# Kernel tuning notes

Measured on AMD Instinct MI355X. Metric: run time of the kernel, lower is better.

Reference implementation:

```python
import jax, jax.numpy as jnp
import numpy as np
from jax import lax

G = 128          # graphs per batch
N_PER = 512      # nodes per graph (uniform -> static top-k shapes)
N = G * N_PER    # 65536 total nodes
E = 1_048_576    # total edges (8192 per graph)
IN, D, OUT = 256, 128, 16
BN_EPS = 1e-5


def setup_inputs() -> dict:
    key = jax.random.key(0)
    ks = jax.random.split(key, 20)
    e_per = E // G
    off = (jnp.arange(G, dtype=jnp.int32) * N_PER)[:, None]
    src = (off + jax.random.randint(ks[0], (G, e_per), 0, N_PER, dtype=jnp.int32)).reshape(-1)
    dst = (off + jax.random.randint(ks[1], (G, e_per), 0, N_PER, dtype=jnp.int32)).reshape(-1)
    inp = {
        "x": jax.random.normal(ks[2], (N, IN), dtype=jnp.float32),
        "edge_index": jnp.stack([src, dst]),
        "batch": jnp.repeat(jnp.arange(G, dtype=jnp.int32), N_PER),
        # GraphConv1: lin_rel (with bias) + lin_root (no bias)
        "w_rel1": jax.random.normal(ks[3], (IN, D)) / np.sqrt(IN),
        "b_rel1": jnp.zeros((D,), jnp.float32),
        "w_root1": jax.random.normal(ks[4], (IN, D)) / np.sqrt(IN),
        "pool1_w": jax.random.normal(ks[5], (D,)) / np.sqrt(D),
        "w_rel2": jax.random.normal(ks[6], (D, D)) / np.sqrt(D),
        "b_rel2": jnp.zeros((D,), jnp.float32),
        "w_root2": jax.random.normal(ks[7], (D, D)) / np.sqrt(D),
        "pool2_w": jax.random.normal(ks[8], (D,)) / np.sqrt(D),
        "lin1_w": jax.random.normal(ks[9], (2 * D, D)) / np.sqrt(2 * D),
        "lin1_b": jnp.zeros((D,), jnp.float32),
        "bn_gamma": jnp.ones((D,), jnp.float32),
        "bn_beta": jnp.zeros((D,), jnp.float32),
        "bn_mean": jnp.zeros((D,), jnp.float32),
        "bn_var": jnp.ones((D,), jnp.float32),
        "lin2_w": jax.random.normal(ks[10], (D, OUT)) / np.sqrt(D),
        "lin2_b": jnp.zeros((OUT,), jnp.float32),
    }
    return inp


def _graph_conv(x, src, dst, valid, w_rel, b_rel, w_root):
    # PyG GraphConv (aggr='add'): lin_rel(sum_{j in N(i)} x_j) + lin_root(x_i)
    msgs = jnp.where(valid[:, None], x[src], 0.0)           # [E, F]
    agg = jax.ops.segment_sum(msgs, dst, num_segments=x.shape[0])
    return agg @ w_rel + b_rel + x @ w_root


def _topk_pool(x, src, dst, valid, w, n_per):
    # PyG TopKPooling: score = sigmoid(x.w / ||w||); keep top ceil(ratio*n) per graph
    k = (n_per + 1) // 2  # ceil(0.5 * n_per)
    score = jax.nn.sigmoid((x @ w) / jnp.sqrt(jnp.sum(w * w)))  # [G*n_per]
    idx_local = lax.top_k(score.reshape(G, n_per), k)[1]        # [G, k]
    perm = (jnp.arange(G, dtype=src.dtype)[:, None] * n_per + idx_local.astype(src.dtype)).reshape(-1)
    x_new = x[perm] * score[perm][:, None]
    # relabel edges (filter_adj): keep edges with both endpoints selected
    mapping = jnp.full((G * n_per,), -1, dtype=src.dtype).at[perm].set(
        jnp.arange(G * k, dtype=src.dtype))
    ns, nd = mapping[src], mapping[dst]
    v = valid & (ns >= 0) & (nd >= 0)
    return x_new, jnp.where(v, ns, 0), jnp.where(v, nd, 0), v, score[perm], k


def _global_pools(x, k):
    xg = x.reshape(G, k, -1)
    return jnp.concatenate([xg.max(axis=1), xg.mean(axis=1)], axis=1)  # [G, 2D]


def reference(x, edge_index, batch, w_rel1, b_rel1, w_root1, pool1_w,
              w_rel2, b_rel2, w_root2, pool2_w, lin1_w, lin1_b,
              bn_gamma, bn_beta, bn_mean, bn_var, lin2_w, lin2_b):
    src, dst = edge_index[0], edge_index[1]
    valid = jnp.ones_like(src, dtype=bool)

    h = jax.nn.relu(_graph_conv(x, src, dst, valid, w_rel1, b_rel1, w_root1))
    h, s1, d1, v1, score_1, k1 = _topk_pool(h, src, dst, valid, pool1_w, N_PER)
    x1 = _global_pools(h, k1)

    h = jax.nn.relu(_graph_conv(h, s1, d1, v1, w_rel2, b_rel2, w_root2))
    h, _, _, _, _, k2 = _topk_pool(h, s1, d1, v1, pool2_w, k1)
    x2 = _global_pools(h, k2)

    g_emb = x1 + x2                                  # [G, 2D]
    z = jax.nn.relu(g_emb @ lin1_w + lin1_b)
    z = (z - bn_mean) * bn_gamma / jnp.sqrt(bn_var + BN_EPS) + bn_beta  # BN (eval)
    # dropout is identity in eval mode
    out = jax.nn.log_softmax(z @ lin2_w + lin2_b, axis=-1)
    return out, g_emb, pool1_w, score_1
```

## Files before the change

### kernel.cpp

```cpp
#include <hip/hip_runtime.h>
#include <cmath>

#define NG    128
#define NPER  512
#define NTOT  65536
#define NEDGE 1048576
#define EPG   8192
#define DD    128
#define K1    256
#define K2    128
#define SLOTS 56

typedef float f32x4 __attribute__((ext_vector_type(4)));
typedef short short8 __attribute__((ext_vector_type(8)));

__device__ __forceinline__ int SW(int row, int c) { return (c ^ ((row >> 1) & 3)) * 8; }

__device__ __forceinline__ void bsplit(float v, short& h, short& l) {
  unsigned u = __builtin_bit_cast(unsigned, v);
  h = (short)(u >> 16);
  float lf = v - __builtin_bit_cast(float, u & 0xFFFF0000u);
  l = (short)(__builtin_bit_cast(unsigned, lf) >> 16);
}

__device__ __forceinline__ void gload16(const void* g, void* l) {
  __builtin_amdgcn_global_load_lds(
      (const __attribute__((address_space(1))) unsigned int*)g,
      (__attribute__((address_space(3))) unsigned int*)l, 16, 0, 0);
}

__global__ __launch_bounds__(256) void build_wt_all(
    const float* __restrict__ W1, const float* __restrict__ W2,
    const float* __restrict__ W3, const float* __restrict__ W4,
    const float* __restrict__ pw1, const float* __restrict__ pw2,
    short* __restrict__ h1, short* __restrict__ l1,
    short* __restrict__ h2, short* __restrict__ l2,
    int* __restrict__ cnt, float* __restrict__ norms) {
  const int n = blockIdx.x, k = threadIdx.x;
  cnt[n * 256 + k] = 0;
  const int t = k >> 5, k5 = k & 31, cq = k5 >> 3, i = k5 & 7;
  const int nhalf = n >> 7, nf = (n >> 4) & 7, l = n & 15;
  const int off = ((((t * 2 + nhalf) * 8 + nf) * 4 + cq) * 16 + l) * 8 + i;
  {
    float w = (nhalf == 0) ? W1[k * 128 + n] : W2[k * 128 + (n - 128)];
    short h, lo; bsplit(w, h, lo);
    h1[off] = h; l1[off] = lo;
  }
  if (k < 128) {
    float w = (nhalf == 0) ? W3[k * 128 + n] : W4[k * 128 + (n - 128)];
    short h, lo; bsplit(w, h, lo);
    h2[off] = h; l2[off] = lo;
  }
  if (n == 0) {
    const int lane = k & 63, wid = k >> 6;
    if (wid < 2 && lane < 32) {
      const float* pw = (wid == 0) ? pw1 : pw2;
      f32x4 wv = *(const f32x4*)&pw[lane * 4];
      float nr = wv[0]*wv[0] + wv[1]*wv[1] + wv[2]*wv[2] + wv[3]*wv[3];
#pragma unroll
      for (int m = 16; m >= 1; m >>= 1) nr += __shfl_xor(nr, m);
      if (lane == 0) norms[wid] = sqrtf(nr);
    }
  }
}

template<int K, int MT>
__global__ __launch_bounds__(256, 2) void gemm_mfma_dual(
    const float* __restrict__ A,
    const short* __restrict__ wth, const short* __restrict__ wtl,
    float* __restrict__ C1, float* __restrict__ C2) {
  constexpr int MF = MT / 32;
  constexpr int NP = MT / 32;
  constexpr int NT = K / 32;
  __shared__ short Ah[MT * 32], Al[MT * 32];
  __shared__ short WHL[2][16384];
  const int tid = threadIdx.x, lane = tid & 63, wid = tid >> 6;
  const int wm = (wid >> 1) * (MT / 2);
  const int nhalf = wid & 1;
  const size_t row0 = (size_t)blockIdx.x * MT;
  const int l15 = lane & 15, cq = lane >> 4;
  const int wfrag = nhalf * 4096 + cq * 128 + l15 * 8;
  const int ar  = (MT == 128) ? (tid >> 1) : (tid >> 2);
  const int cb0 = (MT == 128) ? ((tid & 1) * 2) : (tid & 3);
  const float* ap = A + (row0 + ar) * K + cb0 * 8;

  float4 pa[NP];
  auto load_a = [&](int t) {
    const float4* p = (const float4*)(ap + t * 32);
#pragma unroll
    for (int i = 0; i < NP; ++i) pa[i] = p[i];
  };
  auto store_a = [&]() {
#pragma unroll
    for (int c = 0; c < NP / 2; ++c) {
      float ff[8] = {pa[2*c].x, pa[2*c].y, pa[2*c].z, pa[2*c].w,
                     pa[2*c+1].x, pa[2*c+1].y, pa[2*c+1].z, pa[2*c+1].w};
      short8 hv, lv;
#pragma unroll
      for (int i = 0; i < 8; ++i) {
        short hh, ll; bsplit(ff[i], hh, ll); hv[i] = hh; lv[i] = ll;
      }
      *(short8*)&Ah[ar * 32 + SW(ar, cb0 + c)] = hv;
      *(short8*)&Al[ar * 32 + SW(ar, cb0 + c)] = lv;
    }
  };
  auto stage_w = [&](int t, int b) {
#pragma unroll
    for (int j = 0; j < 8; ++j) {
      int c = wid * 8 + j;
      const short* gs = (c < 16) ? wth + (size_t)t * 8192 + c * 512 + lane * 8
                                 : wtl + (size_t)t * 8192 + (c - 16) * 512 + lane * 8;
      gload16(gs, &WHL[b][c * 512 + lane * 8]);
    }
  };

  f32x4 acc[MF][8];
#pragma unroll
  for (int mf = 0; mf < MF; ++mf)
#pragma unroll
    for (int nf = 0; nf < 8; ++nf) acc[mf][nf] = (f32x4){0.f, 0.f, 0.f, 0.f};

  load_a(0);
  stage_w(0, 0);
  store_a();
  __syncthreads();
  int cur = 0;

  for (int t = 0; t < NT; ++t) {
    if (t + 1 < NT) {
      load_a(t + 1);
      stage_w(t + 1, cur ^ 1);
    }
    short8 ah[MF], al[MF];
#pragma unroll
    for (int mf = 0; mf < MF; ++mf) {
      int r = wm + mf * 16 + l15;
      ah[mf] = *(const short8*)&Ah[r * 32 + SW(r, cq)];
      al[mf] = *(const short8*)&Al[r * 32 + SW(r, cq)];
    }
#pragma unroll
    for (int nf = 0; nf < 8; ++nf) {
      short8 bh = *(const short8*)&WHL[cur][nf * 512 + wfrag];
      short8 bl = *(const short8*)&WHL[cur][8192 + nf * 512 + wfrag];
#pragma unroll
      for (int mf = 0; mf < MF; ++mf) {
        acc[mf][nf] = __builtin_amdgcn_mfma_f32_16x16x32_bf16(ah[mf], bh, acc[mf][nf], 0, 0, 0);
        acc[mf][nf] = __builtin_amdgcn_mfma_f32_16x16x32_bf16(ah[mf], bl, acc[mf][nf], 0, 0, 0);
        acc[mf][nf] = __builtin_amdgcn_mfma_f32_16x16x32_bf16(al[mf], bh, acc[mf][nf], 0, 0, 0);
      }
    }
    if (t + 1 < NT) {
      __syncthreads();
      store_a();
      __syncthreads();
      cur ^= 1;
    }
  }

  float* Cb = nhalf ? C2 : C1;
#pragma unroll
  for (int mf = 0; mf < MF; ++mf) {
    size_t rbase = row0 + wm + mf * 16 + cq * 4;
#pragma unroll
    for (int nf = 0; nf < 8; ++nf) {
      int c = nf * 16 + l15;
#pragma unroll
      for (int r = 0; r < 4; ++r)
        Cb[(rbase + r) * 128 + c] = acc[mf][nf][r];
    }
  }
}

__global__ __launch_bounds__(512) void bucket_fill1(
    const int* __restrict__ src, const int* __restrict__ dst,
    int* __restrict__ cnt, int* __restrict__ eid) {
  int e = blockIdx.x * 512 + threadIdx.x;
  int d = dst[e];
  int pos = atomicAdd(&cnt[d], 1);
  eid[d * SLOTS + pos] = src[e];
}

__global__ __launch_bounds__(512) void bucket_fill2(
    const int* __restrict__ src, const int* __restrict__ dst,
    const int* __restrict__ map, int* __restrict__ cnt, int* __restrict__ eid) {
  int e = blockIdx.x * 512 + threadIdx.x;
  int ms = map[src[e]], md = map[dst[e]];
  if ((ms | md) >= 0) {
    int pos = atomicAdd(&cnt[md], 1);
    eid[md * SLOTS + pos] = ms;
  }
}

template<int CPX>
__global__ __launch_bounds__(64) void agg_gather(
    const float* __restrict__ xr, const float* __restrict__ xo,
    const float* __restrict__ brel, const int* __restrict__ cnt,
    const int* __restrict__ eid, const float* __restrict__ pw,
    const float* __restrict__ wnorm_p,
    float* __restrict__ hout, float* __restrict__ score) {
  const int bid = blockIdx.x;
  const int node = (bid & 7) * CPX + (bid >> 3);
  const int lane = threadIdx.x;
  const int dg = cnt[node];
  const int base = node * SLOTS;
  const int half = lane >> 5, l32 = lane & 31;
  const int eall = eid[base + lane];
  const float wnorm = wnorm_p[0];
  f32x4 a0 = {0.f, 0.f, 0.f, 0.f}, a1 = a0, a2 = a0, a3 = a0;
  int j = 0;
  for (; j + 8 <= dg; j += 8) {
    int e0 = __shfl(eall, j + 0 + half);
    int e1 = __shfl(eall, j + 2 + half);
    int e2 = __shfl(eall, j + 4 + half);
    int e3 = __shfl(eall, j + 6 + half);
    a0 += *(const f32x4*)&xr[(size_t)e0 * 128 + l32 * 4];
    a1 += *(const f32x4*)&xr[(size_t)e1 * 128 + l32 * 4];
    a2 += *(const f32x4*)&xr[(size_t)e2 * 128 + l32 * 4];
    a3 += *(const f32x4*)&xr[(size_t)e3 * 128 + l32 * 4];
  }
  if (j + 4 <= dg) {
    int e0 = __shfl(eall, j + 0 + half);
    int e1 = __shfl(eall, j + 2 + half);
    a0 += *(const f32x4*)&xr[(size_t)e0 * 128 + l32 * 4];
    a1 += *(const f32x4*)&xr[(size_t)e1 * 128 + l32 * 4];
    j += 4;
  }
  if (j + 2 <= dg) {
    int e0 = __shfl(eall, j + half);
    a2 += *(const f32x4*)&xr[(size_t)e0 * 128 + l32 * 4];
    j += 2;
  }
  {
    int e0 = __shfl(eall, j);
    if (j < dg && half == 0)
      a3 += *(const f32x4*)&xr[(size_t)e0 * 128 + l32 * 4];
  }
  f32x4 s = a0 + a1 + a2 + a3;
  s[0] += __shfl_xor(s[0], 32);
  s[1] += __shfl_xor(s[1], 32);
  s[2] += __shfl_xor(s[2], 32);
  s[3] += __shfl_xor(s[3], 32);
  float dot = 0.f;
  if (half == 0) {
    const f32x4 wv = *(const f32x4*)&pw[l32 * 4];
    f32x4 b = *(const f32x4*)&brel[l32 * 4];
    f32x4 o = *(const f32x4*)&xo[(size_t)node * 128 + l32 * 4];
    f32x4 h;
#pragma unroll
    for (int i = 0; i < 4; ++i) {
      h[i] = fmaxf(s[i] + b[i] + o[i], 0.f);
      dot += h[i] * wv[i];
    }
    *(f32x4*)&hout[(size_t)node * 128 + l32 * 4] = h;
  }
#pragma unroll
  for (int m = 16; m >= 1; m >>= 1) dot += __shfl_xor(dot, m);
  if (lane == 0)
    score[node] = 1.f / (1.f + expf(-dot / wnorm));
}

__global__ __launch_bounds__(512) void topk1_kernel(
    const float* __restrict__ h1, const float* __restrict__ score_in,
    float* __restrict__ xnew, int* __restrict__ map, int* __restrict__ cnt,
    float* __restrict__ x1p, float* __restrict__ score_out) {
  const int g = blockIdx.x, tid = threadIdx.x;
  __shared__ float sc[NPER];
  __shared__ int si[NPER];
  __shared__ float xn[K1 * 128];
  __shared__ float redm[4 * 128];
  __shared__ float reds[4 * 128];
  {
    int gt = g * 512 + tid;
    if (gt < NG * K1) cnt[gt] = 0;
  }
  sc[tid] = score_in[g * NPER + tid];
  si[tid] = tid;

  for (int k = 2; k <= NPER; k <<= 1) {
    for (int j = k >> 1; j > 0; j >>= 1) {
      __syncthreads();
      int p = tid ^ j;
      if (p > tid) {
        float sa = sc[tid], sb = sc[p];
        int ia = si[tid], ib = si[p];
        bool before = (sb > sa) || (sb == sa && ib < ia);
        if (before == ((tid & k) == 0)) {
          sc[tid] = sb; sc[p] = sa; si[tid] = ib; si[p] = ia;
        }
      }
    }
  }
  __syncthreads();

  map[g * NPER + tid] = -1;
  if (tid < K1) score_out[g * K1 + tid] = sc[tid];
  __syncthreads();
  if (tid < K1) map[g * NPER + si[tid]] = g * K1 + tid;

  const int wave = tid >> 6, lane = tid & 63;
  for (int j = wave; j < K1; j += 8) {
    int idx = si[j];
    float s2 = sc[j];
    float2 v = *(const float2*)&h1[(size_t)(g * NPER + idx) * 128 + lane * 2];
    float2 o;
    o.x = v.x * s2;
    o.y = v.y * s2;
    *(float2*)&xnew[(size_t)(g * K1 + j) * 128 + lane * 2] = o;
    xn[j * 128 + lane * 2] = o.x;
    xn[j * 128 + lane * 2 + 1] = o.y;
  }
  __syncthreads();

  const int c = tid & 127, grp = tid >> 7;
  float mx = -1e30f, sm = 0.f;
  for (int r = grp; r < K1; r += 4) {
    float v = xn[r * 128 + c];
    mx = fmaxf(mx, v);
    sm += v;
  }
  redm[grp * 128 + c] = mx;
  reds[grp * 128 + c] = sm;
  __syncthreads();
  if (tid < 128) {
    float m = fmaxf(fmaxf(redm[c], redm[128 + c]), fmaxf(redm[256 + c], redm[384 + c]));
    float su = reds[c] + reds[128 + c] + reds[256 + c] + reds[384 + c];
    x1p[g * 256 + tid] = m;
    x1p[g * 256 + 128 + tid] = su * (1.f / 256.f);
  }
}

__global__ __launch_bounds__(256) void topk2_head_kernel(
    const float* __restrict__ h2, const float* __restrict__ score_in,
    const float* __restrict__ x1p,
    const float* __restrict__ lin1_w, const float* __restrict__ lin1_b,
    const float* __restrict__ bng, const float* __restrict__ bnb,
    const float* __restrict__ bnm, const float* __restrict__ bnv,
    const float* __restrict__ lin2_w, const float* __restrict__ lin2_b,
    const float* __restrict__ pool1_w, float* __restrict__ out) {
  const int g = blockIdx.x, tid = threadIdx.x;
  __shared__ float sc[K1];
  __shared__ int si[K1];
  __shared__ float xn[K2 * 128];
  __shared__ float redm[2 * 128];
  __shared__ float reds[2 * 128];
  __shared__ float ge[256];
  __shared__ float zz[128];
  __shared__ float lg[16];
  sc[tid] = score_in[g * K1 + tid];
  si[tid] = tid;
  for (int k = 2; k <= K1; k <<= 1) {
    for (int j = k >> 1; j > 0; j >>= 1) {
      __syncthreads();
      int p = tid ^ j;
      if (p > tid) {
        float sa = sc[tid], sb = sc[p];
        int ia = si[tid], ib = si[p];
        bool before = (sb > sa) || (sb == sa && ib < ia);
        if (before == ((tid & k) == 0)) {
          sc[tid] = sb; sc[p] = sa; si[tid] = ib; si[p] = ia;
        }
      }
    }
  }
  __syncthreads();
  const int wave = tid >> 6, lane = tid & 63;
  for (int j = wave; j < K2; j += 4) {
    int idx = si[j];
    float s2 = sc[j];
    float2 v = *(const float2*)&h2[(size_t)(g * K1 + idx) * 128 + lane * 2];
    xn[j * 128 + lane * 2] = v.x * s2;
    xn[j * 128 + lane * 2 + 1] = v.y * s2;
  }
  __syncthreads();
  const int c = tid & 127, grp = tid >> 7;
  float mx = -1e30f, sm = 0.f;
  for (int r = grp; r < K2; r += 2) {
    float v = xn[r * 128 + c];
    mx = fmaxf(mx, v);
    sm += v;
  }
  redm[grp * 128 + c] = mx;
  reds[grp * 128 + c] = sm;
  __syncthreads();
  if (tid < 128) {
    float m = fmaxf(redm[c], redm[128 + c]);
    float su = (reds[c] + reds[128 + c]) * (1.f / 128.f);
    float v1 = x1p[g * 256 + tid] + m;
    float v2 = x1p[g * 256 + 128 + tid] + su;
    ge[tid] = v1;
    ge[128 + tid] = v2;
    out[2048 + g * 256 + tid] = v1;
    out[2048 + g * 256 + 128 + tid] = v2;
  }
  __syncthreads();
  if (tid < 128) {
    float a = lin1_b[tid];
    for (int k = 0; k < 256; ++k) a += ge[k] * lin1_w[k * 128 + tid];
    a = fmaxf(a, 0.f);
    a = (a - bnm[tid]) * bng[tid] / sqrtf(bnv[tid] + 1e-5f) + bnb[tid];
    zz[tid] = a;
  }
  __syncthreads();
  if (tid < 16) {
    float o = lin2_b[tid];
    for (int k = 0; k < 128; ++k) o += zz[k] * lin2_w[k * 16 + tid];
    lg[tid] = o;
  }
  __syncthreads();
  if (tid < 16) {
    float m = lg[0];
    for (int j = 1; j < 16; ++j) m = fmaxf(m, lg[j]);
    float ssum = 0.f;
    for (int j = 0; j < 16; ++j) ssum += expf(lg[j] - m);
    out[g * 16 + tid] = lg[tid] - m - logf(ssum);
  }
  if (g == 0 && tid < 128) out[34816 + tid] = pool1_w[tid];
}

extern "C" void kernel_launch(void* const* d_in, const int* in_sizes, int n_in,
                              void* d_out, int out_size, void* d_ws, size_t ws_size,
                              hipStream_t stream) {
  const float* x       = (const float*)d_in[0];
  const int*   ei      = (const int*)d_in[1];
  const float* w_rel1  = (const float*)d_in[3];
  const float* b_rel1  = (const float*)d_in[4];
  const float* w_root1 = (const float*)d_in[5];
  const float* pool1_w = (const float*)d_in[6];
  const float* w_rel2  = (const float*)d_in[7];
  const float* b_rel2  = (const float*)d_in[8];
  const float* w_root2 = (const float*)d_in[9];
  const float* pool2_w = (const float*)d_in[10];
  const float* lin1_w  = (const float*)d_in[11];
  const float* lin1_b  = (const float*)d_in[12];
  const float* bng     = (const float*)d_in[13];
  const float* bnb     = (const float*)d_in[14];
  const float* bnm     = (const float*)d_in[15];
  const float* bnv     = (const float*)d_in[16];
  const float* lin2_w  = (const float*)d_in[17];
  const float* lin2_b  = (const float*)d_in[18];
  const int* src = ei;
  const int* dst = ei + NEDGE;

  char* ws = (char*)d_ws;
  float* xr1  = (float*)(ws + 0);
  float* xoh1 = (float*)(ws + 33554432UL);
  float* xnew = (float*)(ws + 67108864UL);
  int*   eid  = (int*)  (ws + 67108864UL);
  int*   map  = (int*)  (ws + 83886080UL);
  int*   cnt  = (int*)  (ws + 84148224UL);
  float* x1p  = (float*)(ws + 84410368UL);
  float* sc1  = (float*)(ws + 84541440UL);
  float* sc2  = (float*)(ws + 84803584UL);
  short* wth1 = (short*)(ws + 84934656UL);
  short* wtl1 = (short*)(ws + 85065728UL);
  short* wth2 = (short*)(ws + 85196800UL);
  short* wtl2 = (short*)(ws + 85262336UL);
  float* norms = (float*)(ws + 85327872UL);
  float* xr2  = (float*)(ws + 0);
  float* xo2  = (float*)(ws + 16777216UL);
  float* h2   = xoh1;
  float* out  = (float*)d_out;

  build_wt_all<<<dim3(256), dim3(256), 0, stream>>>(
      w_rel1, w_root1, w_rel2, w_root2, pool1_w, pool2_w,
      wth1, wtl1, wth2, wtl2, cnt, norms);
  gemm_mfma_dual<256, 128><<<dim3(512), dim3(256), 0, stream>>>(x, wth1, wtl1, xr1, xoh1);
  bucket_fill1<<<dim3(NEDGE / 512), dim3(512), 0, stream>>>(src, dst, cnt, eid);
  agg_gather<8192><<<dim3(NTOT), dim3(64), 0, stream>>>(
      xr1, xoh1, b_rel1, cnt, eid, pool1_w, norms, xoh1, sc1);
  topk1_kernel<<<dim3(NG), dim3(512), 0, stream>>>(xoh1, sc1, xnew, map, cnt, x1p, out + 34944);

  gemm_mfma_dual<128, 64><<<dim3(512), dim3(256), 0, stream>>>(xnew, wth2, wtl2, xr2, xo2);
  bucket_fill2<<<dim3(NEDGE / 512), dim3(512), 0, stream>>>(src, dst, map, cnt, eid);
  agg_gather<4096><<<dim3(NG * K1), dim3(64), 0, stream>>>(
      xr2, xo2, b_rel2, cnt, eid, pool2_w, norms + 1, h2, sc2);

  topk2_head_kernel<<<dim3(NG), dim3(K1), 0, stream>>>(h2, sc2, x1p,
      lin1_w, lin1_b, bng, bnb, bnm, bnv, lin2_w, lin2_b, pool1_w, out);
}
```

Before: 177.4 us.

## Fuse edge bucket fill into the dual GEMM kernels' prologue

Removes the separate bucket_fill1 and bucket_fill2 launches. Each of the two GEMM blocks now first scatters 2048 edges into the per-node slot buckets with atomics, then runs its MFMA GEMM. The aim is to drop two kernel launches and hide the latency-bound atomic scatter behind GEMM work running in other blocks. Because the second fill now runs alongside the GEMM that reads xnew, its bucket buffer moves to a separate workspace region (the free upper part of xoh1) so it cannot overwrite the GEMM input. The cost is more work in the GEMM prologue before its loads can start.

```diff
diff --git a/kernel.cpp b/kernel.cpp
--- a/kernel.cpp
+++ b/kernel.cpp
@@ -64,17 +64,38 @@
   }
 }
 
-template<int K, int MT>
-__global__ __launch_bounds__(256, 2) void gemm_mfma_dual(
+template<int K, int MT, bool FILL2>
+__global__ __launch_bounds__(256, 2) void gemm_fill(
     const float* __restrict__ A,
     const short* __restrict__ wth, const short* __restrict__ wtl,
-    float* __restrict__ C1, float* __restrict__ C2) {
+    float* __restrict__ C1, float* __restrict__ C2,
+    const int* __restrict__ esrc, const int* __restrict__ edst,
+    const int* __restrict__ map, int* __restrict__ cnt, int* __restrict__ eid) {
   constexpr int MF = MT / 32;
   constexpr int NP = MT / 32;
   constexpr int NT = K / 32;
   __shared__ short Ah[MT * 32], Al[MT * 32];
   __shared__ short WHL[2][16384];
   const int tid = threadIdx.x, lane = tid & 63, wid = tid >> 6;
+
+  {
+#pragma unroll
+    for (int i = 0; i < 8; ++i) {
+      int e = blockIdx.x * 2048 + i * 256 + tid;
+      if (!FILL2) {
+        int d = edst[e];
+        int pos = atomicAdd(&cnt[d], 1);
+        eid[d * SLOTS + pos] = esrc[e];
+      } else {
+        int ms = map[esrc[e]], md = map[edst[e]];
+        if ((ms | md) >= 0) {
+          int pos = atomicAdd(&cnt[md], 1);
+          eid[md * SLOTS + pos] = ms;
+        }
+      }
+    }
+  }
+
   const int wm = (wid >> 1) * (MT / 2);
   const int nhalf = wid & 1;
   const size_t row0 = (size_t)blockIdx.x * MT;
@@ -168,26 +189,6 @@
       for (int r = 0; r < 4; ++r)
         Cb[(rbase + r) * 128 + c] = acc[mf][nf][r];
     }
-  }
-}
-
-__global__ __launch_bounds__(512) void bucket_fill1(
-    const int* __restrict__ src, const int* __restrict__ dst,
-    int* __restrict__ cnt, int* __restrict__ eid) {
-  int e = blockIdx.x * 512 + threadIdx.x;
-  int d = dst[e];
-  int pos = atomicAdd(&cnt[d], 1);
-  eid[d * SLOTS + pos] = src[e];
-}
-
-__global__ __launch_bounds__(512) void bucket_fill2(
-    const int* __restrict__ src, const int* __restrict__ dst,
-    const int* __restrict__ map, int* __restrict__ cnt, int* __restrict__ eid) {
-  int e = blockIdx.x * 512 + threadIdx.x;
-  int ms = map[src[e]], md = map[dst[e]];
-  if ((ms | md) >= 0) {
-    int pos = atomicAdd(&cnt[md], 1);
-    eid[md * SLOTS + pos] = ms;
   }
 }
 
@@ -445,7 +446,8 @@
   float* xr1  = (float*)(ws + 0);
   float* xoh1 = (float*)(ws + 33554432UL);
   float* xnew = (float*)(ws + 67108864UL);
-  int*   eid  = (int*)  (ws + 67108864UL);
+  int*   eid1 = (int*)  (ws + 67108864UL);
+  int*   eid2 = (int*)  (ws + 50331648UL);
   int*   map  = (int*)  (ws + 83886080UL);
   int*   cnt  = (int*)  (ws + 84148224UL);
   float* x1p  = (float*)(ws + 84410368UL);
@@ -464,16 +466,16 @@
   build_wt_all<<<dim3(256), dim3(256), 0, stream>>>(
       w_rel1, w_root1, w_rel2, w_root2, pool1_w, pool2_w,
       wth1, wtl1, wth2, wtl2, cnt, norms);
-  gemm_mfma_dual<256, 128><<<dim3(512), dim3(256), 0, stream>>>(x, wth1, wtl1, xr1, xoh1);
-  bucket_fill1<<<dim3(NEDGE / 512), dim3(512), 0, stream>>>(src, dst, cnt, eid);
+  gemm_fill<256, 128, false><<<dim3(512), dim3(256), 0, stream>>>(
+      x, wth1, wtl1, xr1, xoh1, src, dst, nullptr, cnt, eid1);
   agg_gather<8192><<<dim3(NTOT), dim3(64), 0, stream>>>(
-      xr1, xoh1, b_rel1, cnt, eid, pool1_w, norms, xoh1, sc1);
+      xr1, xoh1, b_rel1, cnt, eid1, pool1_w, norms, xoh1, sc1);
   topk1_kernel<<<dim3(NG), dim3(512), 0, stream>>>(xoh1, sc1, xnew, map, cnt, x1p, out + 34944);
 
-  gemm_mfma_dual<128, 64><<<dim3(512), dim3(256), 0, stream>>>(xnew, wth2, wtl2, xr2, xo2);
-  bucket_fill2<<<dim3(NEDGE / 512), dim3(512), 0, stream>>>(src, dst, map, cnt, eid);
+  gemm_fill<128, 64, true><<<dim3(512), dim3(256), 0, stream>>>(
+      xnew, wth2, wtl2, xr2, xo2, src, dst, map, cnt, eid2);
   agg_gather<4096><<<dim3(NG * K1), dim3(64), 0, stream>>>(
-      xr2, xo2, b_rel2, cnt, eid, pool2_w, norms + 1, h2, sc2);
+      xr2, xo2, b_rel2, cnt, eid2, pool2_w, norms + 1, h2, sc2);
 
   topk2_head_kernel<<<dim3(NG), dim3(K1), 0, stream>>>(h2, sc2, x1p,
       lin1_w, lin1_b, bng, bnb, bnm, bnv, lin2_w, lin2_b, pool1_w, out);
```

Measured after the change: 165.9 us. 6.5% less time.
